# Kernel optimization log

Hardware: AMD Instinct MI355X
Metric: run time of the kernel (lower is better)

Reference implementation:

```python
import jax, jax.numpy as jnp
import numpy as np

EPS = 1e-8

def dice(x, alpha):
    # Dice activation (dim=3): per-channel BN (batch stats over B,L axes), then gating.
    m = jnp.mean(x, axis=(0, 1), keepdims=True)
    v = jnp.var(x, axis=(0, 1), keepdims=True)
    p = jax.nn.sigmoid((x - m) * jax.lax.rsqrt(v + EPS))
    return p * x + (1.0 - p) * alpha * x


def setup_inputs() -> dict:
    key = jax.random.key(0)
    ks = jax.random.split(key, 12)
    B, L, D = 2048, 200, 128
    H1, H2 = 128, 32
    query = jax.random.normal(ks[0], (B, D), dtype=jnp.float32)
    keys = jax.random.normal(ks[1], (B, L, D), dtype=jnp.float32)
    keys_len = jax.random.randint(ks[2], (B,), 0, L)
    s1 = 1.0 / np.sqrt(4 * D)
    s2 = 1.0 / np.sqrt(H1)
    s3 = 1.0 / np.sqrt(H2)
    W1 = jax.random.uniform(ks[3], (4 * D, H1), minval=-s1, maxval=s1, dtype=jnp.float32)
    b1 = jax.random.uniform(ks[4], (H1,), minval=-s1, maxval=s1, dtype=jnp.float32)
    alpha1 = jnp.zeros((H1,), dtype=jnp.float32)
    W2 = jax.random.uniform(ks[5], (H1, H2), minval=-s2, maxval=s2, dtype=jnp.float32)
    b2 = jax.random.uniform(ks[6], (H2,), minval=-s2, maxval=s2, dtype=jnp.float32)
    alpha2 = jnp.zeros((H2,), dtype=jnp.float32)
    Wd = jax.random.uniform(ks[7], (H2, 1), minval=-s3, maxval=s3, dtype=jnp.float32)
    bd = jax.random.uniform(ks[8], (1,), minval=-s3, maxval=s3, dtype=jnp.float32)
    return {"query": query, "keys": keys, "keys_len": keys_len,
            "W1": W1, "b1": b1, "alpha1": alpha1,
            "W2": W2, "b2": b2, "alpha2": alpha2,
            "Wd": Wd, "bd": bd}


def reference(query, keys, keys_len, W1, b1, alpha1, W2, b2, alpha2, Wd, bd):
    B, L, D = keys.shape
    q = jnp.broadcast_to(query[:, None, :], (B, L, D))
    # concat/diff/product features -> (B, L, 4D)
    x = jnp.concatenate([q, keys, q - keys, q * keys], axis=-1)
    h = dice(x @ W1 + b1, alpha1)
    h = dice(h @ W2 + b2, alpha2)
    score = (h @ Wd + bd)[..., 0]            # (B, L)
    mask = jnp.arange(L) < keys_len[:, None]  # (B, L)
    score = jnp.where(mask, score, 0.0)
    # weighted-sum pooling: (B, L) x (B, L, D) -> (B, D)
    return jnp.einsum('bl,bld->bd', score, keys)
```

## Files before the change

### kernel.cpp

```cpp
#include <hip/hip_runtime.h>
#include <hip/hip_bf16.h>
#include <stdint.h>

typedef __attribute__((ext_vector_type(8))) short bf16x8;
typedef __attribute__((ext_vector_type(8))) unsigned short u16x8;
typedef __attribute__((ext_vector_type(4))) float f32x4;

#define B_SZ 2048
#define L_SZ 200
#define D_SZ 128
#define NROWS (B_SZ * L_SZ)
#define NTILES (NROWS / 16)

__device__ __forceinline__ short f2bf(float f) {
    __bf16 h = (__bf16)f;
    return __builtin_bit_cast(short, h);
}
__device__ __forceinline__ float bf2f(short s) {
    union { uint32_t u; float f; } v; v.u = ((uint32_t)(uint16_t)s) << 16;
    return v.f;
}
__device__ __forceinline__ float sigm(float x) {
    return 1.0f / (1.0f + __expf(-x));
}

__global__ void k0_prep(const float* __restrict__ W1, const float* __restrict__ W2,
                        float* __restrict__ Aprime, float* __restrict__ Bf32,
                        float* __restrict__ Cf32, ushort* __restrict__ W2f,
                        float* __restrict__ stats)
{
    const int total = 16384 + 16384 + 16384 + 4096 + 512;
    for (int i = blockIdx.x * blockDim.x + threadIdx.x; i < total; i += gridDim.x * blockDim.x) {
        if (i < 16384) {
            int r = i >> 7, c = i & 127;
            Aprime[i] = W1[r * 128 + c] + W1[(256 + r) * 128 + c];
        } else if (i < 32768) {
            int e = i - 16384;
            int j = e & 7, l = (e >> 3) & 63, kt = (e >> 9) & 3, ct = e >> 11;
            int k = kt * 32 + ((l >> 4) << 3) + j;
            int col = (ct << 4) + (l & 15);
            Bf32[e] = W1[(128 + k) * 128 + col] - W1[(256 + k) * 128 + col];
        } else if (i < 49152) {
            int e = i - 32768;
            int j = e & 7, l = (e >> 3) & 63, kt = (e >> 9) & 3, ct = e >> 11;
            int k = kt * 32 + ((l >> 4) << 3) + j;
            int col = (ct << 4) + (l & 15);
            Cf32[e] = W1[(384 + k) * 128 + col];
        } else if (i < 49152 + 4096) {
            int f = i - 49152;
            int j = f & 7, l = (f >> 3) & 63, kt = (f >> 9) & 3, ct = f >> 11;
            int kk = kt * 32 + ((l >> 4) << 3) + j;
            int col = (ct << 4) + (l & 15);
            W2f[f] = (ushort)f2bf(W2[kk * 32 + col]);
        } else {
            stats[i - (49152 + 4096)] = 0.0f;
        }
    }
}

__global__ void k1_qA(const float* __restrict__ q, const float* __restrict__ Aprime,
                      const float* __restrict__ b1, float* __restrict__ qA)
{
    __shared__ float qs[128];
    int b = blockIdx.x, c = threadIdx.x;
    qs[c] = q[b * 128 + c];
    __syncthreads();
    float acc = b1[c];
    #pragma unroll 8
    for (int r = 0; r < 128; ++r) acc += qs[r] * Aprime[r * 128 + c];
    qA[b * 128 + c] = acc;
}

__global__ void __launch_bounds__(64, 4) k2_main(
    const float* __restrict__ query, const float* __restrict__ keys,
    const float* __restrict__ qA, const float* __restrict__ Bf32,
    const float* __restrict__ Cf32, ushort* __restrict__ z1,
    float* __restrict__ stats1)
{
    const int p = blockIdx.x;
    const int b = (p & 7) | ((p >> 5) << 3);
    const int cg = (p >> 3) & 3;
    const int lane = threadIdx.x;
    const int r15 = lane & 15, g = lane >> 4;

    f32x4 qv[4][2];
    #pragma unroll
    for (int kt = 0; kt < 4; ++kt) {
        const float* qp = query + (size_t)b * 128 + kt * 32 + g * 8;
        qv[kt][0] = *(const f32x4*)(qp);
        qv[kt][1] = *(const f32x4*)(qp + 4);
    }

    bf16x8 wb[2][4];
    #pragma unroll
    for (int ctl = 0; ctl < 2; ++ctl)
        #pragma unroll
        for (int kt = 0; kt < 4; ++kt) {
            const int ct = cg * 2 + ctl;
            const int fi = ((ct * 4 + kt) * 64 + lane) * 8;
            f32x4 b0 = *(const f32x4*)(Bf32 + fi);
            f32x4 b1v = *(const f32x4*)(Bf32 + fi + 4);
            f32x4 c0 = *(const f32x4*)(Cf32 + fi);
            f32x4 c1 = *(const f32x4*)(Cf32 + fi + 4);
            bf16x8 w;
            #pragma unroll
            for (int j = 0; j < 4; ++j) {
                w[j]     = f2bf(b0[j]  + qv[kt][0][j] * c0[j]);
                w[4 + j] = f2bf(b1v[j] + qv[kt][1][j] * c1[j]);
            }
            wb[ctl][kt] = w;
        }

    float qa[2];
    #pragma unroll
    for (int ctl = 0; ctl < 2; ++ctl)
        qa[ctl] = qA[(size_t)b * 128 + (cg * 2 + ctl) * 16 + r15];

    float ssum[2] = {0, 0}, ssq[2] = {0, 0};

    const float* kbase = keys + (size_t)b * L_SZ * 128;
    ushort* zbase = z1 + (size_t)b * L_SZ * 128;

    for (int t = 0; t < 13; ++t) {
        const int row0 = t * 16;
        const int lrowc = min(row0 + r15, L_SZ - 1);
        const float* kp = kbase + (size_t)lrowc * 128 + g * 8;

        bf16x8 afr[4];
        #pragma unroll
        for (int kt = 0; kt < 4; ++kt) {
            f32x4 k0 = *(const f32x4*)(kp + kt * 32);
            f32x4 k1 = *(const f32x4*)(kp + kt * 32 + 4);
            bf16x8 a;
            #pragma unroll
            for (int j = 0; j < 4; ++j) { a[j] = f2bf(k0[j]); a[4 + j] = f2bf(k1[j]); }
            afr[kt] = a;
        }

        f32x4 acc[2];
        #pragma unroll
        for (int ctl = 0; ctl < 2; ++ctl) {
            acc[ctl] = (f32x4){0, 0, 0, 0};
            #pragma unroll
            for (int kt = 0; kt < 4; ++kt)
                acc[ctl] = __builtin_amdgcn_mfma_f32_16x16x32_bf16(afr[kt], wb[ctl][kt], acc[ctl], 0, 0, 0);
        }

        const int rbase = row0 + g * 4;
        #pragma unroll
        for (int j = 0; j < 4; ++j) {
            const int row = rbase + j;
            if (row < L_SZ) {
                #pragma unroll
                for (int ctl = 0; ctl < 2; ++ctl) {
                    float v = acc[ctl][j] + qa[ctl];
                    ssum[ctl] += v;
                    ssq[ctl] += v * v;
                    zbase[(size_t)row * 128 + (cg * 2 + ctl) * 16 + r15] = (ushort)f2bf(v);
                }
            }
        }
    }

    #pragma unroll
    for (int ctl = 0; ctl < 2; ++ctl) {
        float s = ssum[ctl], q2 = ssq[ctl];
        s += __shfl_xor(s, 16); s += __shfl_xor(s, 32);
        q2 += __shfl_xor(q2, 16); q2 += __shfl_xor(q2, 32);
        if (g == 0) {
            const int col = (cg * 2 + ctl) * 16 + r15;
            atomicAdd(&stats1[col], s);
            atomicAdd(&stats1[128 + col], q2);
        }
    }
}

__global__ void k_fin(const float* __restrict__ raw, float* __restrict__ fin, int nch)
{
    int c = threadIdx.x;
    if (c >= nch) return;
    float n = (float)NROWS;
    float m = raw[c] / n;
    float v = raw[nch + c] / n - m * m;
    float r = rsqrtf(v + 1e-8f);
    fin[c] = r;
    fin[nch + c] = -m * r;
}

__global__ void __launch_bounds__(64, 2) k4_z2(
    const ushort* __restrict__ z1, const ushort* __restrict__ W2f,
    const float* __restrict__ fin1, const float* __restrict__ alpha1,
    const float* __restrict__ b2, ushort* __restrict__ z2, float* __restrict__ stats2)
{
    const int lane = threadIdx.x, r15 = lane & 15, g = lane >> 4;
    bf16x8 bfr[2][4];
    #pragma unroll
    for (int ct = 0; ct < 2; ++ct)
        #pragma unroll
        for (int kt = 0; kt < 4; ++kt)
            bfr[ct][kt] = *(const bf16x8*)(W2f + ((size_t)(ct * 4 + kt) * 64 + lane) * 8);

    f32x4 rstd4[4][2], bias4[4][2], alp4[4][2];
    #pragma unroll
    for (int kt = 0; kt < 4; ++kt) {
        const int base = kt * 32 + g * 8;
        rstd4[kt][0] = *(const f32x4*)(fin1 + base);
        rstd4[kt][1] = *(const f32x4*)(fin1 + base + 4);
        bias4[kt][0] = *(const f32x4*)(fin1 + 128 + base);
        bias4[kt][1] = *(const f32x4*)(fin1 + 128 + base + 4);
        alp4[kt][0]  = *(const f32x4*)(alpha1 + base);
        alp4[kt][1]  = *(const f32x4*)(alpha1 + base + 4);
    }
    float b2v[2] = { b2[r15], b2[16 + r15] };
    float ssum[2] = {0, 0}, ssq[2] = {0, 0};

    for (int rt = blockIdx.x; rt < NTILES; rt += gridDim.x) {
        int rowA = rt * 16 + r15;
        bf16x8 afr[4];
        #pragma unroll
        for (int kt = 0; kt < 4; ++kt) {
            bf16x8 zv = *(const bf16x8*)(z1 + (size_t)rowA * 128 + kt * 32 + g * 8);
            bf16x8 hv;
            #pragma unroll
            for (int jj = 0; jj < 8; ++jj) {
                const int h = jj >> 2, j = jj & 3;
                float z = bf2f(zv[jj]);
                float zh = z * rstd4[kt][h][j] + bias4[kt][h][j];
                float pgate = sigm(zh);
                float t = pgate + (1.0f - pgate) * alp4[kt][h][j];
                hv[jj] = f2bf(z * t);
            }
            afr[kt] = hv;
        }
        f32x4 acc[2];
        #pragma unroll
        for (int ct = 0; ct < 2; ++ct) {
            acc[ct] = (f32x4){0, 0, 0, 0};
            #pragma unroll
            for (int kt = 0; kt < 4; ++kt)
                acc[ct] = __builtin_amdgcn_mfma_f32_16x16x32_bf16(afr[kt], bfr[ct][kt], acc[ct], 0, 0, 0);
        }
        int rowC = rt * 16 + g * 4;
        #pragma unroll
        for (int j = 0; j < 4; ++j) {
            int row = rowC + j;
            #pragma unroll
            for (int ct = 0; ct < 2; ++ct) {
                float v = acc[ct][j] + b2v[ct];
                ssum[ct] += v;
                ssq[ct] += v * v;
                z2[(size_t)row * 32 + ct * 16 + r15] = (ushort)f2bf(v);
            }
        }
    }
    #pragma unroll
    for (int ct = 0; ct < 2; ++ct) {
        float s = ssum[ct], q2 = ssq[ct];
        s += __shfl_xor(s, 16); s += __shfl_xor(s, 32);
        q2 += __shfl_xor(q2, 16); q2 += __shfl_xor(q2, 32);
        if (g == 0) {
            int col = ct * 16 + r15;
            atomicAdd(&stats2[col], s);
            atomicAdd(&stats2[32 + col], q2);
        }
    }
}

__global__ void __launch_bounds__(256) k6_score_pool(
    const ushort* __restrict__ z2, const float* __restrict__ keys,
    const int* __restrict__ keys_len, const float* __restrict__ fin2,
    const float* __restrict__ alpha2, const float* __restrict__ Wd,
    const float* __restrict__ bd, float* __restrict__ out)
{
    __shared__ float pp[129];
    __shared__ float sc[200];
    __shared__ float part[2][128];
    int b = blockIdx.x, t = threadIdx.x;
    if (t < 64) pp[t] = fin2[t];
    else if (t < 96) pp[t] = alpha2[t - 64];
    else if (t < 128) pp[t] = Wd[t - 96];
    else if (t == 128) pp[128] = bd[0];
    __syncthreads();

    int klen = keys_len[b];
    if (t < 200) {
        float s = 0.0f;
        if (t < klen) {
            const ushort* zp = z2 + ((size_t)b * 200 + t) * 32;
            u16x8 zr[4];
            #pragma unroll
            for (int i = 0; i < 4; ++i) zr[i] = ((const u16x8*)zp)[i];
            s = pp[128];
            #pragma unroll
            for (int c = 0; c < 32; ++c) {
                float z = bf2f((short)zr[c >> 3][c & 7]);
                float zh = z * pp[c] + pp[32 + c];
                float pg = sigm(zh);
                float h = z * (pg + (1.0f - pg) * pp[64 + c]);
                s += h * pp[96 + c];
            }
        }
        sc[t] = s;
    }
    __syncthreads();

    int c = t & 127, prt = t >> 7;
    int lim = min(100, klen - prt * 100);
    const float* kp = keys + ((size_t)b * 200 + prt * 100) * 128 + c;
    float acc = 0.0f;
    #pragma unroll 4
    for (int l = 0; l < lim; ++l) acc += sc[prt * 100 + l] * kp[(size_t)l * 128];
    part[prt][c] = acc;
    __syncthreads();
    if (t < 128) out[(size_t)b * 128 + t] = part[0][t] + part[1][t];
}

extern "C" void kernel_launch(void* const* d_in, const int* in_sizes, int n_in,
                              void* d_out, int out_size, void* d_ws, size_t ws_size,
                              hipStream_t stream) {
    const float* query    = (const float*)d_in[0];
    const float* keys     = (const float*)d_in[1];
    const int*   keys_len = (const int*)d_in[2];
    const float* W1       = (const float*)d_in[3];
    const float* b1       = (const float*)d_in[4];
    const float* alpha1   = (const float*)d_in[5];
    const float* W2       = (const float*)d_in[6];
    const float* b2       = (const float*)d_in[7];
    const float* alpha2   = (const float*)d_in[8];
    const float* Wd       = (const float*)d_in[9];
    const float* bd       = (const float*)d_in[10];
    float* out = (float*)d_out;

    char* ws = (char*)d_ws;
    ushort* z1     = (ushort*)(ws);
    ushort* z2     = (ushort*)(ws + 104857600);
    float*  qA     = (float*)(ws + 131072000);
    float*  Aprime = (float*)(ws + 132120576);
    float*  Bf32   = (float*)(ws + 132186112);
    float*  Cf32   = (float*)(ws + 132251648);
    ushort* W2f    = (ushort*)(ws + 132317184);
    float*  stats  = (float*)(ws + 132325376);
    float*  fin1   = (float*)(ws + 132327424);
    float*  fin2   = (float*)(ws + 132328448);

    k0_prep<<<128, 256, 0, stream>>>(W1, W2, Aprime, Bf32, Cf32, W2f, stats);
    k1_qA<<<B_SZ, 128, 0, stream>>>(query, Aprime, b1, qA);
    k2_main<<<8192, 64, 0, stream>>>(query, keys, qA, Bf32, Cf32, z1, stats);
    k_fin<<<1, 128, 0, stream>>>(stats, fin1, 128);
    k4_z2<<<5120, 64, 0, stream>>>(z1, W2f, fin1, alpha1, b2, z2, stats + 256);
    k_fin<<<1, 32, 0, stream>>>(stats + 256, fin2, 32);
    k6_score_pool<<<B_SZ, 256, 0, stream>>>(z2, keys, keys_len, fin2, alpha2, Wd, bd, out);
}
```

Baseline: 313.1 us.

## Merge column-group waves per batch and stage MFMA outputs through LDS for vector stores

k2_main now launches one 256-thread block per batch, with four waves each covering a 32-column group, so the four waves share the same keys rows through cache. Both k2_main and k4_z2 write MFMA results into a per-wave LDS staging tile and then emit 16-byte vectorized global stores instead of scattered 2-byte stores. k4_z2 also moves W2 fragments and BN/alpha parameters into shared memory, loaded once per 256-thread block, to reduce register pressure and raise occupancy. The cost is extra LDS traffic and changed occupancy bounds.

```diff
diff --git a/kernel.cpp b/kernel.cpp
--- a/kernel.cpp
+++ b/kernel.cpp
@@ -71,16 +71,17 @@
     qA[b * 128 + c] = acc;
 }
 
-__global__ void __launch_bounds__(64, 4) k2_main(
+__global__ void __launch_bounds__(256, 8) k2_main(
     const float* __restrict__ query, const float* __restrict__ keys,
     const float* __restrict__ qA, const float* __restrict__ Bf32,
     const float* __restrict__ Cf32, ushort* __restrict__ z1,
     float* __restrict__ stats1)
 {
-    const int p = blockIdx.x;
-    const int b = (p & 7) | ((p >> 5) << 3);
-    const int cg = (p >> 3) & 3;
-    const int lane = threadIdx.x;
+    __shared__ ushort stg[4][512];
+    const int tid = threadIdx.x;
+    const int lane = tid & 63;
+    const int cg = tid >> 6;
+    const int b = blockIdx.x;
     const int r15 = lane & 15, g = lane >> 4;
 
     f32x4 qv[4][2];
@@ -120,6 +121,7 @@
 
     const float* kbase = keys + (size_t)b * L_SZ * 128;
     ushort* zbase = z1 + (size_t)b * L_SZ * 128;
+    ushort* sp = stg[cg];
 
     for (int t = 0; t < 13; ++t) {
         const int row0 = t * 16;
@@ -146,19 +148,22 @@
                 acc[ctl] = __builtin_amdgcn_mfma_f32_16x16x32_bf16(afr[kt], wb[ctl][kt], acc[ctl], 0, 0, 0);
         }
 
-        const int rbase = row0 + g * 4;
         #pragma unroll
         for (int j = 0; j < 4; ++j) {
-            const int row = rbase + j;
-            if (row < L_SZ) {
-                #pragma unroll
-                for (int ctl = 0; ctl < 2; ++ctl) {
-                    float v = acc[ctl][j] + qa[ctl];
-                    ssum[ctl] += v;
-                    ssq[ctl] += v * v;
-                    zbase[(size_t)row * 128 + (cg * 2 + ctl) * 16 + r15] = (ushort)f2bf(v);
-                }
-            }
+            const int row = row0 + g * 4 + j;
+            const bool valid = (row < L_SZ);
+            #pragma unroll
+            for (int ctl = 0; ctl < 2; ++ctl) {
+                float v = acc[ctl][j] + qa[ctl];
+                if (valid) { ssum[ctl] += v; ssq[ctl] += v * v; }
+                sp[(g * 4 + j) * 32 + ctl * 16 + r15] = (ushort)f2bf(v);
+            }
+        }
+
+        const int srow = row0 + (lane >> 2);
+        if (srow < L_SZ) {
+            u16x8 vv = *(const u16x8*)(sp + (lane >> 2) * 32 + (lane & 3) * 8);
+            *(u16x8*)(zbase + (size_t)srow * 128 + cg * 32 + (lane & 3) * 8) = vv;
         }
     }
 
@@ -187,72 +192,76 @@
     fin[nch + c] = -m * r;
 }
 
-__global__ void __launch_bounds__(64, 2) k4_z2(
+__global__ void __launch_bounds__(256, 6) k4_z2(
     const ushort* __restrict__ z1, const ushort* __restrict__ W2f,
     const float* __restrict__ fin1, const float* __restrict__ alpha1,
     const float* __restrict__ b2, ushort* __restrict__ z2, float* __restrict__ stats2)
 {
-    const int lane = threadIdx.x, r15 = lane & 15, g = lane >> 4;
-    bf16x8 bfr[2][4];
-    #pragma unroll
-    for (int ct = 0; ct < 2; ++ct)
-        #pragma unroll
-        for (int kt = 0; kt < 4; ++kt)
-            bfr[ct][kt] = *(const bf16x8*)(W2f + ((size_t)(ct * 4 + kt) * 64 + lane) * 8);
-
-    f32x4 rstd4[4][2], bias4[4][2], alp4[4][2];
-    #pragma unroll
-    for (int kt = 0; kt < 4; ++kt) {
-        const int base = kt * 32 + g * 8;
-        rstd4[kt][0] = *(const f32x4*)(fin1 + base);
-        rstd4[kt][1] = *(const f32x4*)(fin1 + base + 4);
-        bias4[kt][0] = *(const f32x4*)(fin1 + 128 + base);
-        bias4[kt][1] = *(const f32x4*)(fin1 + 128 + base + 4);
-        alp4[kt][0]  = *(const f32x4*)(alpha1 + base);
-        alp4[kt][1]  = *(const f32x4*)(alpha1 + base + 4);
-    }
+    __shared__ ushort w2s[4096];
+    __shared__ float par[384];
+    __shared__ ushort stg[4][512];
+
+    const int tid = threadIdx.x, lane = tid & 63, wid = tid >> 6;
+    for (int i = tid; i < 4096; i += 256) w2s[i] = W2f[i];
+    for (int i = tid; i < 384; i += 256) par[i] = (i < 256) ? fin1[i] : alpha1[i - 256];
+    __syncthreads();
+
+    const int r15 = lane & 15, g = lane >> 4;
     float b2v[2] = { b2[r15], b2[16 + r15] };
     float ssum[2] = {0, 0}, ssq[2] = {0, 0};
-
-    for (int rt = blockIdx.x; rt < NTILES; rt += gridDim.x) {
-        int rowA = rt * 16 + r15;
+    ushort* sp = stg[wid];
+
+    for (int rt = blockIdx.x * 4 + wid; rt < NTILES; rt += gridDim.x * 4) {
+        const int rowA = rt * 16 + r15;
         bf16x8 afr[4];
         #pragma unroll
         for (int kt = 0; kt < 4; ++kt) {
             bf16x8 zv = *(const bf16x8*)(z1 + (size_t)rowA * 128 + kt * 32 + g * 8);
+            const int base = kt * 32 + g * 8;
+            f32x4 r0 = *(const f32x4*)(par + base);
+            f32x4 r1 = *(const f32x4*)(par + base + 4);
+            f32x4 o0 = *(const f32x4*)(par + 128 + base);
+            f32x4 o1 = *(const f32x4*)(par + 128 + base + 4);
+            f32x4 a0 = *(const f32x4*)(par + 256 + base);
+            f32x4 a1 = *(const f32x4*)(par + 256 + base + 4);
             bf16x8 hv;
             #pragma unroll
-            for (int jj = 0; jj < 8; ++jj) {
-                const int h = jj >> 2, j = jj & 3;
-                float z = bf2f(zv[jj]);
-                float zh = z * rstd4[kt][h][j] + bias4[kt][h][j];
-                float pgate = sigm(zh);
-                float t = pgate + (1.0f - pgate) * alp4[kt][h][j];
-                hv[jj] = f2bf(z * t);
+            for (int j = 0; j < 4; ++j) {
+                float zl = bf2f(zv[j]);
+                float pg = sigm(zl * r0[j] + o0[j]);
+                hv[j] = f2bf(zl * (pg + (1.0f - pg) * a0[j]));
+                float zh = bf2f(zv[4 + j]);
+                float ph = sigm(zh * r1[j] + o1[j]);
+                hv[4 + j] = f2bf(zh * (ph + (1.0f - ph) * a1[j]));
             }
             afr[kt] = hv;
         }
+
         f32x4 acc[2];
         #pragma unroll
         for (int ct = 0; ct < 2; ++ct) {
             acc[ct] = (f32x4){0, 0, 0, 0};
             #pragma unroll
-            for (int kt = 0; kt < 4; ++kt)
-                acc[ct] = __builtin_amdgcn_mfma_f32_16x16x32_bf16(afr[kt], bfr[ct][kt], acc[ct], 0, 0, 0);
-        }
-        int rowC = rt * 16 + g * 4;
+            for (int kt = 0; kt < 4; ++kt) {
+                bf16x8 bf = *(const bf16x8*)(w2s + ((ct * 4 + kt) * 64 + lane) * 8);
+                acc[ct] = __builtin_amdgcn_mfma_f32_16x16x32_bf16(afr[kt], bf, acc[ct], 0, 0, 0);
+            }
+        }
+
         #pragma unroll
         for (int j = 0; j < 4; ++j) {
-            int row = rowC + j;
             #pragma unroll
             for (int ct = 0; ct < 2; ++ct) {
                 float v = acc[ct][j] + b2v[ct];
                 ssum[ct] += v;
                 ssq[ct] += v * v;
-                z2[(size_t)row * 32 + ct * 16 + r15] = (ushort)f2bf(v);
-            }
-        }
-    }
+                sp[(g * 4 + j) * 32 + ct * 16 + r15] = (ushort)f2bf(v);
+            }
+        }
+        u16x8 vv = *(const u16x8*)(sp + (lane >> 2) * 32 + (lane & 3) * 8);
+        *(u16x8*)(z2 + ((size_t)rt * 16 + (lane >> 2)) * 32 + (lane & 3) * 8) = vv;
+    }
+
     #pragma unroll
     for (int ct = 0; ct < 2; ++ct) {
         float s = ssum[ct], q2 = ssq[ct];
@@ -345,9 +354,9 @@
 
     k0_prep<<<128, 256, 0, stream>>>(W1, W2, Aprime, Bf32, Cf32, W2f, stats);
     k1_qA<<<B_SZ, 128, 0, stream>>>(query, Aprime, b1, qA);
-    k2_main<<<8192, 64, 0, stream>>>(query, keys, qA, Bf32, Cf32, z1, stats);
+    k2_main<<<B_SZ, 256, 0, stream>>>(query, keys, qA, Bf32, Cf32, z1, stats);
     k_fin<<<1, 128, 0, stream>>>(stats, fin1, 128);
-    k4_z2<<<5120, 64, 0, stream>>>(z1, W2f, fin1, alpha1, b2, z2, stats + 256);
+    k4_z2<<<2048, 256, 0, stream>>>(z1, W2f, fin1, alpha1, b2, z2, stats + 256);
     k_fin<<<1, 32, 0, stream>>>(stats + 256, fin2, 32);
     k6_score_pool<<<B_SZ, 256, 0, stream>>>(z2, keys, keys_len, fin2, alpha2, Wd, bd, out);
 }
```

Result: slower. 504.1 us (+61.0%).
